# Optimization experiments

Measured on AMD Instinct MI355X. Metric: run time of the kernel, lower is better.

The kernel has to match this reference:

```python
import jax, jax.numpy as jnp
import numpy as np

B, L, C = 2, 1024, 512
H, P = 8, 4
D = C // H
LN_EPS = 1e-5


def setup_inputs() -> dict:
    key = jax.random.key(0)
    ks = jax.random.split(key, 12)
    s = 0.02
    inp = {
        "features": jax.random.normal(ks[0], (B, L, C), jnp.float32),
        "coords": jax.random.normal(ks[1], (B, L, 3), jnp.float32),
        # LayerNorm params
        "ln_g": jnp.ones((C,), jnp.float32),
        "ln_b": jnp.zeros((C,), jnp.float32),
        # scalar q/k/v projections (stored as [in, out])
        "wq": jax.random.normal(ks[2], (C, C), jnp.float32) * s,
        "bq": jnp.zeros((C,), jnp.float32),
        "wk": jax.random.normal(ks[3], (C, C), jnp.float32) * s,
        "bk": jnp.zeros((C,), jnp.float32),
        "wv": jax.random.normal(ks[4], (C, C), jnp.float32) * s,
        "bv": jnp.zeros((C,), jnp.float32),
        # point q/k/v projections: [C, H*P*3]
        "wqp": jax.random.normal(ks[5], (C, H * P * 3), jnp.float32) * s,
        "bqp": jnp.zeros((H * P * 3,), jnp.float32),
        "wkp": jax.random.normal(ks[6], (C, H * P * 3), jnp.float32) * s,
        "bkp": jnp.zeros((H * P * 3,), jnp.float32),
        "wvp": jax.random.normal(ks[7], (C, H * P * 3), jnp.float32) * s,
        "bvp": jnp.zeros((H * P * 3,), jnp.float32),
        # output projection
        "wo": jax.random.normal(ks[8], (C, C), jnp.float32) * s,
        "bo": jnp.zeros((C,), jnp.float32),
        # per-head point scale, init 1/sqrt(P)
        "pscale": jnp.full((H,), 1.0 / np.sqrt(P), jnp.float32),
    }
    return inp


def _layernorm(x, g, b):
    mu = jnp.mean(x, axis=-1, keepdims=True)
    var = jnp.mean((x - mu) ** 2, axis=-1, keepdims=True)
    return (x - mu) * jax.lax.rsqrt(var + LN_EPS) * g + b


def reference(features, coords, ln_g, ln_b, wq, bq, wk, bk, wv, bv,
              wqp, bqp, wkp, bkp, wvp, bvp, wo, bo, pscale):
    b, l, c = features.shape
    h = pscale.shape[0]
    d = c // h
    p = wqp.shape[1] // (h * 3)

    x = _layernorm(features, ln_g, ln_b)

    # scalar heads: [b,h,l,d]
    q_s = (x @ wq + bq).reshape(b, l, h, d).transpose(0, 2, 1, 3)
    k_s = (x @ wk + bk).reshape(b, l, h, d).transpose(0, 2, 1, 3)
    v_s = (x @ wv + bv).reshape(b, l, h, d).transpose(0, 2, 1, 3)

    # point heads: [b,h,l,p,3]
    q_p = (x @ wqp + bqp).reshape(b, l, h, p, 3).transpose(0, 2, 1, 3, 4)
    k_p = (x @ wkp + bkp).reshape(b, l, h, p, 3).transpose(0, 2, 1, 3, 4)

    # scalar logits
    logits_s = jnp.einsum('bhid,bhjd->bhij', q_s, k_s) * (d ** -0.5)

    # point-distance logits: sum_{p,k} ||q - k||^2 = |q|^2 + |k|^2 - 2 q.k
    # (avoids materializing the [b,h,l,l,p,3] difference tensor)
    dot = jnp.einsum('bhipk,bhjpk->bhij', q_p, k_p)
    qsq = jnp.sum(q_p * q_p, axis=(-1, -2))  # [b,h,l]
    ksq = jnp.sum(k_p * k_p, axis=(-1, -2))  # [b,h,l]
    pdist2 = qsq[..., :, None] + ksq[..., None, :] - 2.0 * dot  # [b,h,l,l]

    logits = logits_s - pdist2 * pscale[None, :, None, None]

    attn = jax.nn.softmax(logits, axis=-1)  # dropout is identity in eval

    out_s = jnp.einsum('bhij,bhjd->bhid', attn, v_s)
    out_s = out_s.transpose(0, 2, 1, 3).reshape(b, l, c)

    out = out_s @ wo + bo  # out_dropout is identity in eval
    return out
```

## Files before the change

kernel.cpp:

```cpp
#include <hip/hip_runtime.h>
#include <math.h>

#define BB 2
#define LL 1024
#define CCH 512
#define HH 8
#define LN_EPSF 1e-5f

typedef short s16x8 __attribute__((ext_vector_type(8)));
typedef float fx4 __attribute__((ext_vector_type(4)));


__device__ __forceinline__ unsigned short f2bf(float f) {
  unsigned u = __float_as_uint(f);
  unsigned r = (u + 0x7FFFu + ((u >> 16) & 1u)) >> 16;
  return (unsigned short)r;
}
__device__ __forceinline__ float bf2f(unsigned short h) {
  return __uint_as_float(((unsigned)h) << 16);
}
__device__ __forceinline__ s16x8 ldfrag(const unsigned short* p) {
  int4 t = *(const int4*)p;
  return *(s16x8*)&t;
}
__device__ __forceinline__ float ex2(float x) {
  float r;
  asm("v_exp_f32 %0, %1" : "=v"(r) : "v"(x));
  return r;
}

template <int CTRL>
__device__ __forceinline__ float dpp_mov(float x) {
  return __int_as_float(
      __builtin_amdgcn_update_dpp(0, __float_as_int(x), CTRL, 0xF, 0xF, true));
}
__device__ __forceinline__ float red16_sum(float v) {
  v += dpp_mov<0x121>(v);
  v += dpp_mov<0x122>(v);
  v += dpp_mov<0x124>(v);
  v += dpp_mov<0x128>(v);
  return v;
}
__device__ __forceinline__ float red16_max(float v) {
  v = fmaxf(v, dpp_mov<0x121>(v));
  v = fmaxf(v, dpp_mov<0x122>(v));
  v = fmaxf(v, dpp_mov<0x124>(v));
  v = fmaxf(v, dpp_mov<0x128>(v));
  return v;
}
__device__ __forceinline__ float wave_sum(float v) {
  v = red16_sum(v);
  v += __shfl_xor(v, 16);
  v += __shfl_xor(v, 32);
  return v;
}

__global__ __launch_bounds__(256) void prep(
    const float* __restrict__ f, const float* __restrict__ g,
    const float* __restrict__ bta, unsigned short* __restrict__ xh,
    unsigned short* __restrict__ xl, const float* __restrict__ wq,
    const float* __restrict__ wk, const float* __restrict__ wv,
    const float* __restrict__ wo, const float* __restrict__ wqp,
    const float* __restrict__ wkp, unsigned short* __restrict__ wt_h,
    unsigned short* __restrict__ qt, unsigned short* __restrict__ kt_) {
  __shared__ unsigned short lh[64][68];
  __shared__ float red[8];
  const int tid = threadIdx.x;
  const int bxg = blockIdx.x;
  if (bxg < 2048) {
    const int row = bxg;
    const int wave = tid >> 6, lane = tid & 63;
    const float* fr = f + (size_t)row * CCH;
    float2 v = *(const float2*)&fr[tid * 2];
    float s = wave_sum(v.x + v.y);
    if (lane == 0) red[wave] = s;
    __syncthreads();
    float mu = (red[0] + red[1] + red[2] + red[3]) * (1.0f / CCH);
    float dx = v.x - mu, dy = v.y - mu;
    float sq = wave_sum(dx * dx + dy * dy);
    if (lane == 0) red[4 + wave] = sq;
    __syncthreads();
    float var = (red[4] + red[5] + red[6] + red[7]) * (1.0f / CCH);
    float inv = 1.0f / sqrtf(var + LN_EPSF);
    float2 gg = *(const float2*)&g[tid * 2];
    float2 bb = *(const float2*)&bta[tid * 2];
    float ox = dx * inv * gg.x + bb.x;
    float oy = dy * inv * gg.y + bb.y;
    unsigned short h0 = f2bf(ox), h1 = f2bf(oy);
    ushort2 hv; hv.x = h0; hv.y = h1;
    ushort2 lv; lv.x = f2bf(ox - bf2f(h0)); lv.y = f2bf(oy - bf2f(h1));
    const int k0c = tid * 2;
    size_t addr = ((size_t)((row >> 4) * 16 + (k0c >> 5))) * 512 +
                  (((k0c >> 3) & 3) * 16 + (row & 15)) * 8 + (k0c & 7);
    *(ushort2*)&xh[addr] = hv;
    *(ushort2*)&xl[addr] = lv;
  } else if (bxg < 2336) {
    const int bx = bxg - 2048;
    const float* W;
    int Ncols, rowbase, kt, nt;
    if (bx < 256) {
      int mat = bx >> 6, t = bx & 63;
      kt = t >> 3; nt = t & 7; Ncols = 512;
      if (mat == 0) { W = wq; rowbase = 0; }
      else if (mat == 1) { W = wk; rowbase = 512; }
      else if (mat == 2) { W = wv; rowbase = 1024; }
      else { W = wo; rowbase = 1536; }
    } else {
      int r = bx - 256; int mat = r >> 4; int t = r & 15;
      kt = t >> 1; nt = t & 1; Ncols = 96;
      if (mat == 0) { W = wqp; rowbase = 2048; }
      else { W = wkp; rowbase = 2144; }
    }
    const int k0 = kt * 64, n0 = nt * 64;
    const int c = tid & 63;
#pragma unroll
    for (int ii = 0; ii < 16; ++ii) {
      int r = ii * 4 + (tid >> 6);
      float val = (n0 + c < Ncols) ? W[(size_t)(k0 + r) * Ncols + n0 + c] : 0.f;
      lh[r][c] = f2bf(val);
    }
    __syncthreads();
    const int base_nt = (rowbase >> 4) + (n0 >> 4);
    const int base_kt = (k0 >> 5);
#pragma unroll
    for (int cc = 0; cc < 2; ++cc) {
      int ch = cc * 256 + tid;
      int lane2 = ch & 63, ktl = (ch >> 6) & 1, ntl = ch >> 7;
      int l16c = lane2 & 15, quadc = lane2 >> 4;
      if (n0 + ntl * 16 < Ncols) {
        unsigned short th[8] __attribute__((aligned(16)));
#pragma unroll
        for (int jj = 0; jj < 8; ++jj)
          th[jj] = lh[ktl * 32 + quadc * 8 + jj][ntl * 16 + l16c];
        *(int4*)&wt_h[((size_t)((base_nt + ntl) * 16 + base_kt + ktl)) * 512 +
                      lane2 * 8] = *(int4*)th;
      }
    }
  } else {
    const int vb2 = bxg - 2336;
    const int4 zero = {0, 0, 0, 0};
    for (int u = tid; u < 32 * 48; u += 256) {
      int t = u / 48, off = (u - t * 48) * 8;
      int gidx = vb2 * 32 + t;
      unsigned short* dst = (gidx < 1024) ? qt : kt_;
      int rem = gidx & 1023;
      int bh = rem >> 6, lt = rem & 63;
      size_t base = ((size_t)(bh * 64 + lt) * 3 + 2) * 512;
      *(int4*)&dst[base + 128 + off] = zero;
    }
  }
}

template <int MF, int NF, int TERMS>
__device__ __forceinline__ void mfma_core_frag(
    const unsigned short* __restrict__ Ah, const unsigned short* __restrict__ Al,
    const unsigned short* __restrict__ Bt, int mt0, int ntbase, int nt0,
    int ntmax, int ks0, int ks1, fx4 acc[MF][NF]) {
  const int lane = threadIdx.x & 63;
  int bt[NF];
#pragma unroll
  for (int j = 0; j < NF; ++j) {
    int nt = nt0 + j;
    if (nt > ntmax) nt = ntmax;
    bt[j] = ntbase + nt;
  }
#pragma unroll
  for (int i = 0; i < MF; ++i)
#pragma unroll
    for (int j = 0; j < NF; ++j) acc[i][j] = (fx4){0.f, 0.f, 0.f, 0.f};
  for (int ks = ks0; ks < ks1; ++ks) {
    s16x8 ah[MF], al[MF], b[NF];
#pragma unroll
    for (int i = 0; i < MF; ++i) {
      size_t off = ((size_t)((mt0 + i) * 16 + ks)) * 512 + lane * 8;
      ah[i] = ldfrag(&Ah[off]);
      if (TERMS == 2) al[i] = ldfrag(&Al[off]);
    }
#pragma unroll
    for (int j = 0; j < NF; ++j)
      b[j] = ldfrag(&Bt[((size_t)(bt[j] * 16 + ks)) * 512 + lane * 8]);
#pragma unroll
    for (int i = 0; i < MF; ++i)
#pragma unroll
      for (int j = 0; j < NF; ++j) {
        acc[i][j] = __builtin_amdgcn_mfma_f32_16x16x32_bf16(ah[i], b[j], acc[i][j], 0, 0, 0);
        if (TERMS == 2)
          acc[i][j] = __builtin_amdgcn_mfma_f32_16x16x32_bf16(al[i], b[j], acc[i][j], 0, 0, 0);
      }
  }
}

__global__ __launch_bounds__(256, 4) void proj_mfma(
    const unsigned short* __restrict__ xh, const unsigned short* __restrict__ xl,
    const unsigned short* __restrict__ wt_h,
    const float* __restrict__ bq, const float* __restrict__ bk,
    const float* __restrict__ bv, const float* __restrict__ bqp,
    const float* __restrict__ bkp, const float* __restrict__ pscale,
    unsigned short* __restrict__ qt, unsigned short* __restrict__ kt_,
    unsigned short* __restrict__ vth) {
  __shared__ unsigned short vt_lds[64][72];
  const int bx = blockIdx.x;
  const int m0 = blockIdx.y * 64;
  const int tid = threadIdx.x;
  const int wave = __builtin_amdgcn_readfirstlane(tid >> 6);
  const int lane = tid & 63;
  const int quad = lane >> 4, l16 = lane & 15;
  const int mw = m0 + (wave & 1) * 32;
  const int mt0 = mw >> 4;

  if (bx < 16) {
    const bool isq = bx < 8;
    const float* bias = isq ? bq : bk;
    unsigned short* pdst = isq ? qt : kt_;
    const int n0 = (bx & 7) * 64;
    const int nw = n0 + (wave >> 1) * 32;
    fx4 acc[2][2];
    mfma_core_frag<2, 2, 1>(xh, xh, wt_h, mt0, isq ? 0 : 32, nw >> 4, 31, 0, 16, acc);
#pragma unroll
    for (int j = 0; j < 2; ++j) {
      int n = nw + j * 16 + l16;
      int h = n >> 6, d = n & 63;
      float bb = bias[n];
#pragma unroll
      for (int i = 0; i < 2; ++i)
#pragma unroll
        for (int reg = 0; reg < 4; ++reg) {
          int row = mw + i * 16 + quad * 4 + reg;
          int bi = row >> 10, l = row & 1023;
          int bh2 = bi * 8 + h;
          float val = (acc[i][j][reg] + bb) * 0.4246609f;
          size_t tile = ((size_t)(bh2 * 64 + (l >> 4))) * 3 + (d >> 5);
          pdst[tile * 512 + (((d >> 3) & 3) * 16 + (l & 15)) * 8 + (d & 7)] = f2bf(val);
        }
    }
  } else if (bx < 24) {
    const int h = bx - 16;
    const int nw = h * 64 + (wave >> 1) * 32;
    fx4 acc[2][2];
    mfma_core_frag<2, 2, 2>(xh, xl, wt_h, mt0, 64, nw >> 4, 31, 0, 16, acc);
#pragma unroll
    for (int j = 0; j < 2; ++j) {
      int dl = (wave >> 1) * 32 + j * 16 + l16;
      float bb = bv[h * 64 + dl];
#pragma unroll
      for (int i = 0; i < 2; ++i)
#pragma unroll
        for (int reg = 0; reg < 4; ++reg) {
          int lm = (wave & 1) * 32 + i * 16 + quad * 4 + reg;
          vt_lds[lm][dl] = f2bf(acc[i][j][reg] + bb);
        }
    }
    __syncthreads();
    const int b = m0 >> 10, l0 = m0 & 1023;
    const int bh2 = b * 8 + h;
#pragma unroll
    for (int cc = 0; cc < 2; ++cc) {
      int ch = cc * 256 + tid;
      int lane2 = ch & 63, jt = (ch >> 6) & 1, ft = ch >> 7;
      int l16c = lane2 & 15, quadc = lane2 >> 4;
      unsigned short th[8] __attribute__((aligned(16)));
#pragma unroll
      for (int jj = 0; jj < 8; ++jj)
        th[jj] = vt_lds[jt * 32 + quadc * 8 + jj][ft * 16 + l16c];
      size_t tile = ((size_t)(bh2 * 4 + ft)) * 32 + (l0 >> 5) + jt;
      *(int4*)&vth[tile * 512 + lane2 * 8] = *(int4*)th;
    }
  } else {
    const bool isq = bx < 26;
    const float* bias = isq ? bqp : bkp;
    unsigned short* pdst = isq ? qt : kt_;
    const int n0 = (bx & 1) * 64;
    const int nw = n0 + (wave >> 1) * 32;
    fx4 acc[2][2];
    mfma_core_frag<2, 2, 1>(xh, xh, wt_h, mt0, isq ? 128 : 134, nw >> 4, 5, 0, 16, acc);
#pragma unroll
    for (int j = 0; j < 2; ++j) {
      int n = nw + j * 16 + l16;
      bool ok = n < 96;
      int nn = ok ? n : 0;
      int h = nn / 12, c = nn - h * 12;
      float sc = sqrtf(2.8853901f * pscale[h]);
      float bb = bias[nn];
#pragma unroll
      for (int i = 0; i < 2; ++i)
#pragma unroll
        for (int reg = 0; reg < 4; ++reg) {
          int row = mw + i * 16 + quad * 4 + reg;
          int bi = row >> 10, l = row & 1023;
          int bh2 = bi * 8 + h;
          float val = (acc[i][j][reg] + bb) * sc;
          if (ok) {
            int kc = 64 + c;
            size_t tile = ((size_t)(bh2 * 64 + (l >> 4))) * 3 + 2;
            pdst[tile * 512 + (((kc >> 3) & 3) * 16 + (l & 15)) * 8 + (kc & 7)] =
                f2bf(val);
          }
        }
    }
  }
}

__global__ __launch_bounds__(64) void aug_sq(
    unsigned short* __restrict__ qt, unsigned short* __restrict__ kt_) {
  const int bid = blockIdx.x;
  const int which = bid & 1;
  const int lt = (bid >> 1) & 63;
  const int bh = bid >> 7;
  unsigned short* t = which ? kt_ : qt;
  const size_t base = ((size_t)(bh * 64 + lt) * 3 + 2) * 512;
  const int lane = threadIdx.x;
  s16x8 v = ldfrag(&t[base + lane * 8]);
  float s = 0.f;
#pragma unroll
  for (int j = 0; j < 8; ++j) {
    float x = bf2f((unsigned short)v[j]);
    if ((lane >> 4) == 1 && j >= 4) x = 0.f;
    if ((lane >> 4) >= 2) x = 0.f;
    s += x * x;
  }
  float tot = 0.5f * (s + __shfl_xor(s, 16));
  if ((lane >> 4) == 1) {
    unsigned short hi = f2bf(tot);
    unsigned short lo = f2bf(tot - bf2f(hi));
    const unsigned short m1 = 0xBF80;
    ushort4 w;
    if (which) { w.x = hi; w.y = lo; w.z = m1; w.w = m1; }
    else       { w.x = m1; w.y = m1; w.z = hi; w.w = lo; }
    *(ushort4*)&t[base + lane * 8 + 4] = w;
  }
}

__global__ __launch_bounds__(256, 4) void ipa_attn_mfma(
    const unsigned short* __restrict__ qt, const unsigned short* __restrict__ kt_,
    const unsigned short* __restrict__ vth, unsigned short* __restrict__ oh) {
  const int bid = blockIdx.x;
  const int low3 = bid & 7;
  const int slot = bid >> 3;
  const int qtile = slot & 63;
  const int bh = ((slot >> 6) << 3) | low3;
  const int tid = threadIdx.x;
  const int wave = tid >> 6, lane = tid & 63;
  const int quad = lane >> 4, l16 = lane & 15;
  const int kq = wave;
  const int ibase = qtile * 16;

  __shared__ __align__(16) float obufF[4 * 16 * 66];
  __shared__ float mred[4][16], lred[4][16];

  unsigned short* pbw = (unsigned short*)&obufF[wave * 16 * 66];

  s16x8 aq[3];
#pragma unroll
  for (int s = 0; s < 3; ++s)
    aq[s] = ldfrag(&qt[(((size_t)(bh * 64 + qtile)) * 3 + s) * 512 + lane * 8]);

  fx4 o[4];
#pragma unroll
  for (int f = 0; f < 4; ++f) o[f] = (fx4){0.f, 0.f, 0.f, 0.f};
  float m_r[4], l_r[4];
#pragma unroll
  for (int reg = 0; reg < 4; ++reg) { m_r[reg] = -INFINITY; l_r[reg] = 0.f; }

#pragma unroll 1
  for (int c = 0; c < 4; ++c) {
    const int j0 = kq * 256 + c * 64;
    fx4 sa[4];
#pragma unroll
    for (int f = 0; f < 4; ++f) sa[f] = (fx4){0.f, 0.f, 0.f, 0.f};
#pragma unroll
    for (int half = 0; half < 2; ++half) {
      s16x8 bk[2][3];
#pragma unroll
      for (int f = 0; f < 2; ++f)
#pragma unroll
        for (int s = 0; s < 3; ++s)
          bk[f][s] = ldfrag(
              &kt_[(((size_t)(bh * 64 + (j0 >> 4) + half * 2 + f)) * 3 + s) * 512 +
                   lane * 8]);
#pragma unroll
      for (int f = 0; f < 2; ++f)
#pragma unroll
        for (int s = 0; s < 3; ++s)
          sa[half * 2 + f] = __builtin_amdgcn_mfma_f32_16x16x32_bf16(
              aq[s], bk[f][s], sa[half * 2 + f], 0, 0, 0);
    }

#pragma unroll
    for (int reg = 0; reg < 4; ++reg) {
      float z0 = sa[0][reg], z1 = sa[1][reg];
      float z2 = sa[2][reg], z3 = sa[3][reg];
      float mx = red16_max(fmaxf(fmaxf(z0, z1), fmaxf(z2, z3)));
      float mnew = fmaxf(m_r[reg], mx);
      float p0 = ex2(z0 - mnew), p1 = ex2(z1 - mnew);
      float p2 = ex2(z2 - mnew), p3 = ex2(z3 - mnew);
      float alpha = ex2(m_r[reg] - mnew);
      float psum = red16_sum((p0 + p1) + (p2 + p3));
      l_r[reg] = l_r[reg] * alpha + psum;
      m_r[reg] = mnew;
      o[0][reg] *= alpha; o[1][reg] *= alpha; o[2][reg] *= alpha; o[3][reg] *= alpha;
      int rb = (quad * 4 + reg) * 72;
      pbw[rb + l16] = f2bf(p0);
      pbw[rb + 16 + l16] = f2bf(p1);
      pbw[rb + 32 + l16] = f2bf(p2);
      pbw[rb + 48 + l16] = f2bf(p3);
    }
    s16x8 bvh[2][4];
#pragma unroll
    for (int kt2 = 0; kt2 < 2; ++kt2)
#pragma unroll
      for (int f = 0; f < 4; ++f)
        bvh[kt2][f] = ldfrag(
            &vth[(((size_t)(bh * 4 + f)) * 32 + (j0 >> 5) + kt2) * 512 + lane * 8]);
    s16x8 ap0 = ldfrag(&pbw[l16 * 72 + quad * 8]);
    s16x8 ap1 = ldfrag(&pbw[l16 * 72 + 32 + quad * 8]);
#pragma unroll
    for (int f = 0; f < 4; ++f) {
      o[f] = __builtin_amdgcn_mfma_f32_16x16x32_bf16(ap0, bvh[0][f], o[f], 0, 0, 0);
      o[f] = __builtin_amdgcn_mfma_f32_16x16x32_bf16(ap1, bvh[1][f], o[f], 0, 0, 0);
    }
  }
  if (l16 == 0) {
#pragma unroll
    for (int reg = 0; reg < 4; ++reg) {
      mred[wave][quad * 4 + reg] = m_r[reg];
      lred[wave][quad * 4 + reg] = l_r[reg];
    }
  }
#pragma unroll
  for (int f = 0; f < 4; ++f)
#pragma unroll
    for (int reg = 0; reg < 4; ++reg)
      obufF[((size_t)(wave * 16 + quad * 4 + reg)) * 66 + f * 16 + l16] = o[f][reg];
  __syncthreads();

  {
    const int b = bh >> 3, h = bh & 7;
    const int d = wave * 16 + l16;
#pragma unroll
    for (int rr = 0; rr < 4; ++rr) {
      int row = quad * 4 + rr;
      float M = -INFINITY;
#pragma unroll
      for (int p = 0; p < 4; ++p) M = fmaxf(M, mred[p][row]);
      float L = 0.f, val = 0.f;
#pragma unroll
      for (int p = 0; p < 4; ++p) {
        float w = ex2(mred[p][row] - M);
        L += lred[p][row] * w;
        val += obufF[((size_t)(p * 16 + row)) * 66 + d] * w;
      }
      val /= L;
      int m = b * LL + ibase + row;
      int kcol = h * 64 + d;
      size_t tile = ((size_t)(m >> 4)) * 16 + (kcol >> 5);
      oh[tile * 512 + (((kcol >> 3) & 3) * 16 + (m & 15)) * 8 + (kcol & 7)] =
          f2bf(val);
    }
  }
}

__global__ __launch_bounds__(256, 4) void out_proj_mfma(
    const unsigned short* __restrict__ oh,
    const unsigned short* __restrict__ wt_h, const float* __restrict__ bo,
    float* __restrict__ out) {
  const int tid = threadIdx.x;
  const int wave = __builtin_amdgcn_readfirstlane(tid >> 6);
  const int lane = tid & 63;
  const int quad = lane >> 4, l16 = lane & 15;
  const int mw = blockIdx.y * 64 + (wave & 1) * 32;
  const int nw = blockIdx.x * 64 + (wave >> 1) * 32;
  fx4 acc[2][2];
  mfma_core_frag<2, 2, 1>(oh, oh, wt_h, mw >> 4, 96, nw >> 4, 31, 0, 16, acc);
#pragma unroll
  for (int j = 0; j < 2; ++j) {
    int n = nw + j * 16 + l16;
    float bb = bo[n];
#pragma unroll
    for (int i = 0; i < 2; ++i)
#pragma unroll
      for (int reg = 0; reg < 4; ++reg) {
        int row = mw + i * 16 + quad * 4 + reg;
        out[(size_t)row * 512 + n] = acc[i][j][reg] + bb;
      }
  }
}

extern "C" void kernel_launch(void* const* d_in, const int* in_sizes, int n_in,
                              void* d_out, int out_size, void* d_ws, size_t ws_size,
                              hipStream_t stream) {
  (void)in_sizes; (void)n_in; (void)out_size; (void)ws_size;
  const float* features = (const float*)d_in[0];
  const float* ln_g = (const float*)d_in[2];
  const float* ln_b = (const float*)d_in[3];
  const float* wq = (const float*)d_in[4];
  const float* bq = (const float*)d_in[5];
  const float* wk = (const float*)d_in[6];
  const float* bk = (const float*)d_in[7];
  const float* wv = (const float*)d_in[8];
  const float* bv = (const float*)d_in[9];
  const float* wqp = (const float*)d_in[10];
  const float* bqp = (const float*)d_in[11];
  const float* wkp = (const float*)d_in[12];
  const float* bkp = (const float*)d_in[13];
  const float* wo = (const float*)d_in[16];
  const float* bo = (const float*)d_in[17];
  const float* pscale = (const float*)d_in[18];
  float* out = (float*)d_out;

  char* cur = (char*)d_ws;
  const size_t NTOK = (size_t)BB * LL;
  unsigned short* xh = (unsigned short*)cur; cur += NTOK * CCH * 2;
  unsigned short* xl = (unsigned short*)cur; cur += NTOK * CCH * 2;
  unsigned short* wt_h = (unsigned short*)cur; cur += (size_t)2240 * 512 * 2;
  unsigned short* qt = (unsigned short*)cur; cur += (size_t)16 * LL * 96 * 2;
  unsigned short* kt_ = (unsigned short*)cur; cur += (size_t)16 * LL * 96 * 2;
  unsigned short* vth = (unsigned short*)cur; cur += (size_t)16 * 64 * LL * 2;
  unsigned short* oh = (unsigned short*)cur; cur += NTOK * CCH * 2;

  prep<<<dim3(2400), 256, 0, stream>>>(features, ln_g, ln_b, xh, xl, wq, wk, wv,
                                       wo, wqp, wkp, wt_h, qt, kt_);
  proj_mfma<<<dim3(28, 32), 256, 0, stream>>>(xh, xl, wt_h, bq, bk, bv, bqp, bkp,
                                              pscale, qt, kt_, vth);
  aug_sq<<<dim3(2048), 64, 0, stream>>>(qt, kt_);
  ipa_attn_mfma<<<dim3(1024), 256, 0, stream>>>(qt, kt_, vth, oh);
  out_proj_mfma<<<dim3(8, 32), 256, 0, stream>>>(oh, wt_h, bo, out);
}
```

Before: 143.1 us.

## Fuse point-tile zeroing and squared-norm augmentation into point projection epilogue

The point projection blocks now write their outputs to shared memory, compute per-head half squared norms there, and assemble the full augmented K-tile (coordinates, hi/lo norm terms, -1 constants, zero padding) in one coalesced 16-byte store per lane. This removes the separate aug_sq kernel launch and the zeroing blocks in prep, along with their global read-modify-write traffic. Each block now handles all 96 point columns with three N fragments instead of two blocks per matrix, which cuts the grid by two columns and adds LDS usage and a couple of barriers per block.

```diff
diff --git a/kernel.cpp b/kernel.cpp
--- a/kernel.cpp
+++ b/kernel.cpp
@@ -61,8 +61,7 @@
     unsigned short* __restrict__ xl, const float* __restrict__ wq,
     const float* __restrict__ wk, const float* __restrict__ wv,
     const float* __restrict__ wo, const float* __restrict__ wqp,
-    const float* __restrict__ wkp, unsigned short* __restrict__ wt_h,
-    unsigned short* __restrict__ qt, unsigned short* __restrict__ kt_) {
+    const float* __restrict__ wkp, unsigned short* __restrict__ wt_h) {
   __shared__ unsigned short lh[64][68];
   __shared__ float red[8];
   const int tid = threadIdx.x;
@@ -94,7 +93,7 @@
                   (((k0c >> 3) & 3) * 16 + (row & 15)) * 8 + (k0c & 7);
     *(ushort2*)&xh[addr] = hv;
     *(ushort2*)&xl[addr] = lv;
-  } else if (bxg < 2336) {
+  } else {
     const int bx = bxg - 2048;
     const float* W;
     int Ncols, rowbase, kt, nt;
@@ -136,18 +135,6 @@
                       lane2 * 8] = *(int4*)th;
       }
     }
-  } else {
-    const int vb2 = bxg - 2336;
-    const int4 zero = {0, 0, 0, 0};
-    for (int u = tid; u < 32 * 48; u += 256) {
-      int t = u / 48, off = (u - t * 48) * 8;
-      int gidx = vb2 * 32 + t;
-      unsigned short* dst = (gidx < 1024) ? qt : kt_;
-      int rem = gidx & 1023;
-      int bh = rem >> 6, lt = rem & 63;
-      size_t base = ((size_t)(bh * 64 + lt) * 3 + 2) * 512;
-      *(int4*)&dst[base + 128 + off] = zero;
-    }
   }
 }
 
@@ -199,6 +186,8 @@
     unsigned short* __restrict__ qt, unsigned short* __restrict__ kt_,
     unsigned short* __restrict__ vth) {
   __shared__ unsigned short vt_lds[64][72];
+  __shared__ unsigned short pt[64][104];
+  __shared__ float hsum[64][8];
   const int bx = blockIdx.x;
   const int m0 = blockIdx.y * 64;
   const int tid = threadIdx.x;
@@ -266,67 +255,72 @@
       *(int4*)&vth[tile * 512 + lane2 * 8] = *(int4*)th;
     }
   } else {
-    const bool isq = bx < 26;
+    const bool isq = bx == 24;
     const float* bias = isq ? bqp : bkp;
     unsigned short* pdst = isq ? qt : kt_;
-    const int n0 = (bx & 1) * 64;
-    const int nw = n0 + (wave >> 1) * 32;
-    fx4 acc[2][2];
-    mfma_core_frag<2, 2, 1>(xh, xh, wt_h, mt0, isq ? 128 : 134, nw >> 4, 5, 0, 16, acc);
-#pragma unroll
-    for (int j = 0; j < 2; ++j) {
+    const int nw = (wave >> 1) * 48;
+    fx4 acc[2][3];
+    mfma_core_frag<2, 3, 1>(xh, xh, wt_h, mt0, isq ? 128 : 134, nw >> 4, 5, 0, 16, acc);
+#pragma unroll
+    for (int j = 0; j < 3; ++j) {
       int n = nw + j * 16 + l16;
-      bool ok = n < 96;
-      int nn = ok ? n : 0;
-      int h = nn / 12, c = nn - h * 12;
+      int h = n / 12;
       float sc = sqrtf(2.8853901f * pscale[h]);
-      float bb = bias[nn];
+      float bb = bias[n];
 #pragma unroll
       for (int i = 0; i < 2; ++i)
 #pragma unroll
         for (int reg = 0; reg < 4; ++reg) {
-          int row = mw + i * 16 + quad * 4 + reg;
-          int bi = row >> 10, l = row & 1023;
-          int bh2 = bi * 8 + h;
-          float val = (acc[i][j][reg] + bb) * sc;
-          if (ok) {
-            int kc = 64 + c;
-            size_t tile = ((size_t)(bh2 * 64 + (l >> 4))) * 3 + 2;
-            pdst[tile * 512 + (((kc >> 3) & 3) * 16 + (l & 15)) * 8 + (kc & 7)] =
-                f2bf(val);
-          }
+          int lm = (wave & 1) * 32 + i * 16 + quad * 4 + reg;
+          pt[lm][n] = f2bf((acc[i][j][reg] + bb) * sc);
         }
     }
-  }
-}
-
-__global__ __launch_bounds__(64) void aug_sq(
-    unsigned short* __restrict__ qt, unsigned short* __restrict__ kt_) {
-  const int bid = blockIdx.x;
-  const int which = bid & 1;
-  const int lt = (bid >> 1) & 63;
-  const int bh = bid >> 7;
-  unsigned short* t = which ? kt_ : qt;
-  const size_t base = ((size_t)(bh * 64 + lt) * 3 + 2) * 512;
-  const int lane = threadIdx.x;
-  s16x8 v = ldfrag(&t[base + lane * 8]);
-  float s = 0.f;
-#pragma unroll
-  for (int j = 0; j < 8; ++j) {
-    float x = bf2f((unsigned short)v[j]);
-    if ((lane >> 4) == 1 && j >= 4) x = 0.f;
-    if ((lane >> 4) >= 2) x = 0.f;
-    s += x * x;
-  }
-  float tot = 0.5f * (s + __shfl_xor(s, 16));
-  if ((lane >> 4) == 1) {
-    unsigned short hi = f2bf(tot);
-    unsigned short lo = f2bf(tot - bf2f(hi));
-    const unsigned short m1 = 0xBF80;
-    ushort4 w;
-    if (which) { w.x = hi; w.y = lo; w.z = m1; w.w = m1; }
-    else       { w.x = m1; w.y = m1; w.z = hi; w.w = lo; }
-    *(ushort4*)&t[base + lane * 8 + 4] = w;
+    __syncthreads();
+#pragma unroll
+    for (int t2 = 0; t2 < 2; ++t2) {
+      int task = tid * 2 + t2;
+      int row = task >> 3, h = task & 7;
+      float s = 0.f;
+#pragma unroll
+      for (int c = 0; c < 12; ++c) {
+        float x = bf2f(pt[row][h * 12 + c]);
+        s += x * x;
+      }
+      hsum[row][h] = 0.5f * s;
+    }
+    __syncthreads();
+    const int bi = m0 >> 10, l0t = (m0 & 1023) >> 4;
+#pragma unroll
+    for (int it = 0; it < 8; ++it) {
+      int idx = it * 256 + tid;
+      int tile = idx >> 6;
+      int lane2 = idx & 63;
+      int h = tile >> 2, lt = tile & 3;
+      int r = lane2 & 15;
+      int row = lt * 16 + r;
+      int kb = (lane2 >> 4) * 8;
+      unsigned short vals[8] __attribute__((aligned(16)));
+#pragma unroll
+      for (int j = 0; j < 8; ++j) {
+        int kl = kb + j;
+        unsigned short v;
+        if (kl < 12) {
+          v = pt[row][h * 12 + kl];
+        } else if (kl >= 16) {
+          v = 0;
+        } else {
+          float tot = hsum[row][h];
+          unsigned short hi = f2bf(tot);
+          unsigned short lo = f2bf(tot - bf2f(hi));
+          bool sumslot = isq ? (kl >= 14) : (kl < 14);
+          v = sumslot ? ((kl & 1) ? lo : hi) : (unsigned short)0xBF80;
+        }
+        vals[j] = v;
+      }
+      int bh2 = bi * 8 + h;
+      size_t tile_g = ((size_t)(bh2 * 64 + (l0t + lt))) * 3 + 2;
+      *(int4*)&pdst[tile_g * 512 + lane2 * 8] = *(int4*)vals;
+    }
   }
 }
 
@@ -517,11 +511,10 @@
   unsigned short* vth = (unsigned short*)cur; cur += (size_t)16 * 64 * LL * 2;
   unsigned short* oh = (unsigned short*)cur; cur += NTOK * CCH * 2;
 
-  prep<<<dim3(2400), 256, 0, stream>>>(features, ln_g, ln_b, xh, xl, wq, wk, wv,
-                                       wo, wqp, wkp, wt_h, qt, kt_);
-  proj_mfma<<<dim3(28, 32), 256, 0, stream>>>(xh, xl, wt_h, bq, bk, bv, bqp, bkp,
+  prep<<<dim3(2336), 256, 0, stream>>>(features, ln_g, ln_b, xh, xl, wq, wk, wv,
+                                       wo, wqp, wkp, wt_h);
+  proj_mfma<<<dim3(26, 32), 256, 0, stream>>>(xh, xl, wt_h, bq, bk, bv, bqp, bkp,
                                               pscale, qt, kt_, vth);
-  aug_sq<<<dim3(2048), 64, 0, stream>>>(qt, kt_);
   ipa_attn_mfma<<<dim3(1024), 256, 0, stream>>>(qt, kt_, vth, oh);
   out_proj_mfma<<<dim3(8, 32), 256, 0, stream>>>(oh, wt_h, bo, out);
 }
```

Result: no change. 144.2 us (+0.8%).
